# Kernel optimization log

Hardware: AMD Instinct MI355X
Metric: run time of the kernel (lower is better)

The kernel has to match this reference:

```python
import jax, jax.numpy as jnp
import numpy as np

TEMPERATURE = 0.07


def setup_inputs() -> dict:
    key = jax.random.key(0)
    k1, k2 = jax.random.split(key)
    B, D = 8192, 128
    z_i = jax.random.normal(k1, (B, D), dtype=jnp.float32)
    z_j = jax.random.normal(k2, (B, D), dtype=jnp.float32)
    return {"z_i": z_i, "z_j": z_j}


def reference(z_i, z_j):
    B = z_i.shape[0]
    # L2-normalize each embedding (F.normalize with eps=1e-12 clamp)
    def l2norm(x):
        n = jnp.linalg.norm(x, axis=1, keepdims=True)
        return x / jnp.maximum(n, 1e-12)
    reps = jnp.concatenate([l2norm(z_i), l2norm(z_j)], axis=0)  # [2B, D]
    sim = jnp.matmul(reps, reps.T) / TEMPERATURE  # [2B, 2B]
    # NOTE: original code applies CrossEntropyLoss to exp(sim/T) values,
    # i.e. the logits themselves are the exponentiated similarities.
    e = jnp.exp(sim)
    N = 2 * B
    idx = jnp.arange(N)
    # CE with the positive placed first and all non-diagonal entries as logits:
    # loss_i = logsumexp(nondiag row) - positive_logit
    neg_inf = jnp.asarray(-jnp.inf, dtype=e.dtype)
    row_logits = jnp.where(idx[None, :] == idx[:, None], neg_inf, e)  # mask diagonal
    lse = jax.scipy.special.logsumexp(row_logits, axis=1)  # [2B]
    pos_idx = jnp.where(idx < B, idx + B, idx - B)
    pos = e[idx, pos_idx]  # [2B]
    return jnp.mean(lse - pos)
```

## Files before the change

### kernel.cpp

```cpp
#include <hip/hip_runtime.h>
#include <hip/hip_bf16.h>


#define NROWS 16384
#define BHALF 8192
#define DDIM  128
#define TILE  128
#define ROWS_PER_BLOCK 256
#define NSPLIT 8
#define COLS_PER_SPLIT (NROWS / NSPLIT)
#define NITERS (COLS_PER_SPLIT / TILE)
#define LDS_STRIDE 136
#define LOG2E 1.4426950408889634f
#define C_EXP (LOG2E / 0.07f)
#define NEGBIG -1.0e30f

typedef __attribute__((ext_vector_type(8))) short bf16x8;
typedef __attribute__((ext_vector_type(4))) float f32x4;

__device__ inline unsigned short f2bf(float x) {
    unsigned int b = __float_as_uint(x);
    b += 0x7FFFu + ((b >> 16) & 1u);
    return (unsigned short)(b >> 16);
}
__device__ inline float bflo(unsigned int u) { return __uint_as_float(u << 16); }
__device__ inline float bfhi(unsigned int u) { return __uint_as_float(u & 0xFFFF0000u); }

__global__ void norm_kernel(const float* __restrict__ zi, const float* __restrict__ zj,
                            unsigned short* __restrict__ repsB,
                            unsigned short* __restrict__ repsA,
                            float* __restrict__ out) {
    int w = threadIdx.x >> 6;
    int lane = threadIdx.x & 63;
    int row = blockIdx.x * 4 + w;
    const float* src = (row < BHALF) ? (zi + (size_t)row * DDIM)
                                     : (zj + (size_t)(row - BHALF) * DDIM);
    float2 v = ((const float2*)src)[lane];
    float ss = v.x * v.x + v.y * v.y;
    #pragma unroll
    for (int d = 1; d < 64; d <<= 1) ss += __shfl_xor(ss, d, 64);
    float inv = 1.0f / fmaxf(sqrtf(ss), 1e-12f);
    float x = v.x * inv, y = v.y * inv;
    unsigned int pb = (unsigned int)f2bf(x) | ((unsigned int)f2bf(y) << 16);
    unsigned int pa = (unsigned int)f2bf(x * C_EXP) | ((unsigned int)f2bf(y * C_EXP) << 16);
    ((unsigned int*)repsB)[(size_t)row * (DDIM / 2) + lane] = pb;
    ((unsigned int*)repsA)[(size_t)row * (DDIM / 2) + lane] = pa;
    if (blockIdx.x == 0 && threadIdx.x == 0) out[0] = 0.0f;
}

template <bool DIAG>
__device__ __forceinline__ void tile_compute(const unsigned short* lds,
                                             const bf16x8 (&afrag)[4][4],
                                             float (&A1)[4][4], float (&A2)[4][4],
                                             int rowBase, int colBase,
                                             int laneLo, int quad) {
    #pragma unroll
    for (int c8 = 0; c8 < 8; ++c8) {
        bf16x8 bfrag[4];
        int brow = c8 * 16 + laneLo;
        #pragma unroll
        for (int kt = 0; kt < 4; ++kt)
            bfrag[kt] = *(const bf16x8*)(&lds[brow * LDS_STRIDE + kt * 32 + quad * 8]);
        #pragma unroll
        for (int rt = 0; rt < 4; ++rt) {
            f32x4 acc = (f32x4){0.f, 0.f, 0.f, 0.f};
            #pragma unroll
            for (int kt = 0; kt < 4; ++kt)
                acc = __builtin_amdgcn_mfma_f32_16x16x32_bf16(
                    afrag[rt][kt], bfrag[kt], acc, 0, 0, 0);
            #pragma unroll
            for (int rg = 0; rg < 4; ++rg) {
                float a = acc[rg];
                if (DIAG) {
                    int drel = rowBase + rt * 16 + quad * 4 + rg - colBase - laneLo;
                    a = (drel == c8 * 16) ? NEGBIG : a;
                }
                float mn = fminf(a, A1[rt][rg]);
                A2[rt][rg] = fmaxf(A2[rt][rg], mn);
                A1[rt][rg] = fmaxf(A1[rt][rg], a);
            }
        }
    }
}

__global__ __launch_bounds__(256, 2)
void ntx_main(const unsigned short* __restrict__ repsA,
              const unsigned short* __restrict__ repsB,
              float2* __restrict__ part) {
    __shared__ unsigned short lds[TILE * LDS_STRIDE];
    const int tid = threadIdx.x;
    const int w = tid >> 6, lane = tid & 63;
    const int laneLo = lane & 15, quad = lane >> 4;
    const int bx = blockIdx.x, by = blockIdx.y;
    const int rowBase = bx * ROWS_PER_BLOCK + w * 64;

    bf16x8 afrag[4][4];
    #pragma unroll
    for (int rt = 0; rt < 4; ++rt)
        #pragma unroll
        for (int kt = 0; kt < 4; ++kt) {
            int r = rowBase + rt * 16 + laneLo;
            int k = kt * 32 + quad * 8;
            afrag[rt][kt] = *(const bf16x8*)(repsA + (size_t)r * DDIM + k);
        }

    float A1[4][4], A2[4][4];
    #pragma unroll
    for (int rt = 0; rt < 4; ++rt)
        #pragma unroll
        for (int rg = 0; rg < 4; ++rg) { A1[rt][rg] = NEGBIG; A2[rt][rg] = NEGBIG; }

    const int colBase0 = by * COLS_PER_SPLIT;
    const uint4* repsV = (const uint4*)repsB;

    for (int it = 0; it < NITERS; ++it) {
        int colBase = colBase0 + it * TILE;
        __syncthreads();
        #pragma unroll
        for (int i = 0; i < 8; ++i) {
            int idx = tid + i * 256;
            int r = idx >> 4, c = idx & 15;
            uint4 v = repsV[(size_t)(colBase + r) * 16 + c];
            *(uint4*)(&lds[r * LDS_STRIDE + c * 8]) = v;
        }
        __syncthreads();

        if ((rowBase >> 7) == (colBase >> 7))
            tile_compute<true>(lds, afrag, A1, A2, rowBase, colBase, laneLo, quad);
        else
            tile_compute<false>(lds, afrag, A1, A2, rowBase, colBase, laneLo, quad);
    }

    #pragma unroll
    for (int rt = 0; rt < 4; ++rt)
        #pragma unroll
        for (int rg = 0; rg < 4; ++rg) {
            float m1 = A1[rt][rg], m2 = A2[rt][rg];
            #pragma unroll
            for (int d = 1; d < 16; d <<= 1) {
                float m1o = __shfl_xor(m1, d, 64);
                float m2o = __shfl_xor(m2, d, 64);
                m2 = fmaxf(fmaxf(m2, m2o), fminf(m1, m1o));
                m1 = fmaxf(m1, m1o);
            }
            if (laneLo == 0) {
                int gr = rowBase + rt * 16 + quad * 4 + rg;
                part[(size_t)gr * NSPLIT + by] = make_float2(m1, m2);
            }
        }
}

__global__ void finish_kernel(const unsigned short* __restrict__ repsB,
                              const float2* __restrict__ part,
                              float* __restrict__ out) {
    int row = blockIdx.x * 256 + threadIdx.x;
    int prow = (row < BHALF) ? row + BHALF : row - BHALF;
    const uint4* rv = (const uint4*)repsB + (size_t)row * 16;
    const uint4* pv = (const uint4*)repsB + (size_t)prow * 16;
    float dot = 0.0f;
    #pragma unroll
    for (int c = 0; c < 16; ++c) {
        uint4 a = rv[c], b = pv[c];
        dot = fmaf(bflo(a.x), bflo(b.x), dot); dot = fmaf(bfhi(a.x), bfhi(b.x), dot);
        dot = fmaf(bflo(a.y), bflo(b.y), dot); dot = fmaf(bfhi(a.y), bfhi(b.y), dot);
        dot = fmaf(bflo(a.z), bflo(b.z), dot); dot = fmaf(bfhi(a.z), bfhi(b.z), dot);
        dot = fmaf(bflo(a.w), bflo(b.w), dot); dot = fmaf(bfhi(a.w), bfhi(b.w), dot);
    }
    float pos = __builtin_amdgcn_exp2f(dot * C_EXP);

    float M1 = NEGBIG, M2 = NEGBIG;
    #pragma unroll
    for (int k = 0; k < NSPLIT; ++k) {
        float2 p = part[(size_t)row * NSPLIT + k];
        M2 = fmaxf(fmaxf(M2, p.y), fminf(M1, p.x));
        M1 = fmaxf(M1, p.x);
    }
    float e1 = __builtin_amdgcn_exp2f(M1);
    float e2 = __builtin_amdgcn_exp2f(M2);
    float lse = e1 + log1pf(__builtin_amdgcn_exp2f((e2 - e1) * LOG2E));
    float v = lse - pos;

    #pragma unroll
    for (int d = 1; d < 64; d <<= 1) v += __shfl_xor(v, d, 64);
    __shared__ float red[4];
    int lane = threadIdx.x & 63, w = threadIdx.x >> 6;
    if (lane == 0) red[w] = v;
    __syncthreads();
    if (threadIdx.x == 0)
        atomicAdd(out, (red[0] + red[1] + red[2] + red[3]) * (1.0f / NROWS));
}

extern "C" void kernel_launch(void* const* d_in, const int* in_sizes, int n_in,
                              void* d_out, int out_size, void* d_ws, size_t ws_size,
                              hipStream_t stream) {
    const float* zi = (const float*)d_in[0];
    const float* zj = (const float*)d_in[1];
    float* out = (float*)d_out;
    unsigned short* repsB = (unsigned short*)d_ws;
    unsigned short* repsA = repsB + (size_t)NROWS * DDIM;
    float2* part = (float2*)((char*)d_ws + 2 * (size_t)NROWS * DDIM * 2);

    norm_kernel<<<NROWS / 4, 256, 0, stream>>>(zi, zj, repsB, repsA, out);
    ntx_main<<<dim3(NROWS / ROWS_PER_BLOCK, NSPLIT), 256, 0, stream>>>(repsA, repsB, part);
    finish_kernel<<<NROWS / 256, 256, 0, stream>>>(repsB, part, out);
}
```

Measured before the change: 137.5 us.

## Widen column tile, interleave two MFMA chains, fuse positive extraction into main kernel

```diff
diff --git a/kernel.cpp b/kernel.cpp
--- a/kernel.cpp
+++ b/kernel.cpp
@@ -5,7 +5,7 @@
 #define NROWS 16384
 #define BHALF 8192
 #define DDIM  128
-#define TILE  128
+#define TILE  256
 #define ROWS_PER_BLOCK 256
 #define NSPLIT 8
 #define COLS_PER_SPLIT (NROWS / NSPLIT)
@@ -23,8 +23,6 @@
     b += 0x7FFFu + ((b >> 16) & 1u);
     return (unsigned short)(b >> 16);
 }
-__device__ inline float bflo(unsigned int u) { return __uint_as_float(u << 16); }
-__device__ inline float bfhi(unsigned int u) { return __uint_as_float(u & 0xFFFF0000u); }
 
 __global__ void norm_kernel(const float* __restrict__ zi, const float* __restrict__ zj,
                             unsigned short* __restrict__ repsB,
@@ -48,36 +46,47 @@
     if (blockIdx.x == 0 && threadIdx.x == 0) out[0] = 0.0f;
 }
 
-template <bool DIAG>
-__device__ __forceinline__ void tile_compute(const unsigned short* lds,
-                                             const bf16x8 (&afrag)[4][4],
-                                             float (&A1)[4][4], float (&A2)[4][4],
-                                             int rowBase, int colBase,
-                                             int laneLo, int quad) {
-    #pragma unroll
-    for (int c8 = 0; c8 < 8; ++c8) {
-        bf16x8 bfrag[4];
-        int brow = c8 * 16 + laneLo;
-        #pragma unroll
-        for (int kt = 0; kt < 4; ++kt)
-            bfrag[kt] = *(const bf16x8*)(&lds[brow * LDS_STRIDE + kt * 32 + quad * 8]);
+template <int MODE>
+__device__ __forceinline__ void tile_compute(
+    const unsigned short* __restrict__ lds,
+    const bf16x8 (&afrag)[4][4],
+    float (&A1)[4][4], float (&A2)[4][4], float (&POS)[4][4],
+    int rowOff, int laneLo, int quad) {
+    const f32x4 kZ = {0.f, 0.f, 0.f, 0.f};
+    #pragma unroll
+    for (int c8 = 0; c8 < 16; c8 += 2) {
+        bf16x8 ba[4], bb[4];
+        const int browa = c8 * 16 + laneLo;
+        #pragma unroll
+        for (int kt = 0; kt < 4; ++kt) {
+            ba[kt] = *(const bf16x8*)(&lds[browa * LDS_STRIDE + kt * 32 + quad * 8]);
+            bb[kt] = *(const bf16x8*)(&lds[(browa + 16) * LDS_STRIDE + kt * 32 + quad * 8]);
+        }
         #pragma unroll
         for (int rt = 0; rt < 4; ++rt) {
-            f32x4 acc = (f32x4){0.f, 0.f, 0.f, 0.f};
+            f32x4 va = kZ, vb = kZ;
             #pragma unroll
-            for (int kt = 0; kt < 4; ++kt)
-                acc = __builtin_amdgcn_mfma_f32_16x16x32_bf16(
-                    afrag[rt][kt], bfrag[kt], acc, 0, 0, 0);
+            for (int kt = 0; kt < 4; ++kt) {
+                va = __builtin_amdgcn_mfma_f32_16x16x32_bf16(afrag[rt][kt], ba[kt], va, 0, 0, 0);
+                vb = __builtin_amdgcn_mfma_f32_16x16x32_bf16(afrag[rt][kt], bb[kt], vb, 0, 0, 0);
+            }
             #pragma unroll
             for (int rg = 0; rg < 4; ++rg) {
-                float a = acc[rg];
-                if (DIAG) {
-                    int drel = rowBase + rt * 16 + quad * 4 + rg - colBase - laneLo;
-                    a = (drel == c8 * 16) ? NEGBIG : a;
+                float a = va[rg], b = vb[rg];
+                if (MODE) {
+                    int rel = rowOff + rt * 16 + quad * 4 + rg - laneLo;
+                    if (MODE == 1) {
+                        a = (rel == c8 * 16) ? NEGBIG : a;
+                        b = (rel == (c8 + 1) * 16) ? NEGBIG : b;
+                    } else {
+                        POS[rt][rg] = fmaxf(POS[rt][rg], (rel == c8 * 16) ? a : NEGBIG);
+                        POS[rt][rg] = fmaxf(POS[rt][rg], (rel == (c8 + 1) * 16) ? b : NEGBIG);
+                    }
                 }
-                float mn = fminf(a, A1[rt][rg]);
-                A2[rt][rg] = fmaxf(A2[rt][rg], mn);
-                A1[rt][rg] = fmaxf(A1[rt][rg], a);
+                float hi = fmaxf(a, b), lo = fminf(a, b);
+                float t = fminf(A1[rt][rg], hi);
+                A1[rt][rg] = fmaxf(A1[rt][rg], hi);
+                A2[rt][rg] = fmaxf(fmaxf(A2[rt][rg], lo), t);
             }
         }
     }
@@ -86,13 +95,17 @@
 __global__ __launch_bounds__(256, 2)
 void ntx_main(const unsigned short* __restrict__ repsA,
               const unsigned short* __restrict__ repsB,
-              float2* __restrict__ part) {
+              float4* __restrict__ part) {
     __shared__ unsigned short lds[TILE * LDS_STRIDE];
     const int tid = threadIdx.x;
     const int w = tid >> 6, lane = tid & 63;
     const int laneLo = lane & 15, quad = lane >> 4;
     const int bx = blockIdx.x, by = blockIdx.y;
     const int rowBase = bx * ROWS_PER_BLOCK + w * 64;
+    const int rowOff = rowBase & 255;
+
+    const int diagCol = bx * ROWS_PER_BLOCK;
+    const int posCol = (diagCol < BHALF) ? diagCol + BHALF : diagCol - BHALF;
 
     bf16x8 afrag[4][4];
     #pragma unroll
@@ -104,11 +117,13 @@
             afrag[rt][kt] = *(const bf16x8*)(repsA + (size_t)r * DDIM + k);
         }
 
-    float A1[4][4], A2[4][4];
+    float A1[4][4], A2[4][4], POS[4][4];
     #pragma unroll
     for (int rt = 0; rt < 4; ++rt)
         #pragma unroll
-        for (int rg = 0; rg < 4; ++rg) { A1[rt][rg] = NEGBIG; A2[rt][rg] = NEGBIG; }
+        for (int rg = 0; rg < 4; ++rg) {
+            A1[rt][rg] = NEGBIG; A2[rt][rg] = NEGBIG; POS[rt][rg] = NEGBIG;
+        }
 
     const int colBase0 = by * COLS_PER_SPLIT;
     const uint4* repsV = (const uint4*)repsB;
@@ -117,7 +132,7 @@
         int colBase = colBase0 + it * TILE;
         __syncthreads();
         #pragma unroll
-        for (int i = 0; i < 8; ++i) {
+        for (int i = 0; i < 16; ++i) {
             int idx = tid + i * 256;
             int r = idx >> 4, c = idx & 15;
             uint4 v = repsV[(size_t)(colBase + r) * 16 + c];
@@ -125,58 +140,49 @@
         }
         __syncthreads();
 
-        if ((rowBase >> 7) == (colBase >> 7))
-            tile_compute<true>(lds, afrag, A1, A2, rowBase, colBase, laneLo, quad);
+        if (colBase == diagCol)
+            tile_compute<1>(lds, afrag, A1, A2, POS, rowOff, laneLo, quad);
+        else if (colBase == posCol)
+            tile_compute<2>(lds, afrag, A1, A2, POS, rowOff, laneLo, quad);
         else
-            tile_compute<false>(lds, afrag, A1, A2, rowBase, colBase, laneLo, quad);
+            tile_compute<0>(lds, afrag, A1, A2, POS, rowOff, laneLo, quad);
     }
 
     #pragma unroll
     for (int rt = 0; rt < 4; ++rt)
         #pragma unroll
         for (int rg = 0; rg < 4; ++rg) {
-            float m1 = A1[rt][rg], m2 = A2[rt][rg];
+            float m1 = A1[rt][rg], m2 = A2[rt][rg], p = POS[rt][rg];
             #pragma unroll
             for (int d = 1; d < 16; d <<= 1) {
                 float m1o = __shfl_xor(m1, d, 64);
                 float m2o = __shfl_xor(m2, d, 64);
+                float po = __shfl_xor(p, d, 64);
                 m2 = fmaxf(fmaxf(m2, m2o), fminf(m1, m1o));
                 m1 = fmaxf(m1, m1o);
+                p = fmaxf(p, po);
             }
             if (laneLo == 0) {
                 int gr = rowBase + rt * 16 + quad * 4 + rg;
-                part[(size_t)gr * NSPLIT + by] = make_float2(m1, m2);
-            }
-        }
-}
-
-__global__ void finish_kernel(const unsigned short* __restrict__ repsB,
-                              const float2* __restrict__ part,
+                part[(size_t)gr * NSPLIT + by] = make_float4(m1, m2, p, 0.0f);
+            }
+        }
+}
+
+__global__ void finish_kernel(const float4* __restrict__ part,
                               float* __restrict__ out) {
     int row = blockIdx.x * 256 + threadIdx.x;
-    int prow = (row < BHALF) ? row + BHALF : row - BHALF;
-    const uint4* rv = (const uint4*)repsB + (size_t)row * 16;
-    const uint4* pv = (const uint4*)repsB + (size_t)prow * 16;
-    float dot = 0.0f;
-    #pragma unroll
-    for (int c = 0; c < 16; ++c) {
-        uint4 a = rv[c], b = pv[c];
-        dot = fmaf(bflo(a.x), bflo(b.x), dot); dot = fmaf(bfhi(a.x), bfhi(b.x), dot);
-        dot = fmaf(bflo(a.y), bflo(b.y), dot); dot = fmaf(bfhi(a.y), bfhi(b.y), dot);
-        dot = fmaf(bflo(a.z), bflo(b.z), dot); dot = fmaf(bfhi(a.z), bfhi(b.z), dot);
-        dot = fmaf(bflo(a.w), bflo(b.w), dot); dot = fmaf(bfhi(a.w), bfhi(b.w), dot);
-    }
-    float pos = __builtin_amdgcn_exp2f(dot * C_EXP);
-
-    float M1 = NEGBIG, M2 = NEGBIG;
+    float M1 = NEGBIG, M2 = NEGBIG, P = NEGBIG;
     #pragma unroll
     for (int k = 0; k < NSPLIT; ++k) {
-        float2 p = part[(size_t)row * NSPLIT + k];
+        float4 p = part[(size_t)row * NSPLIT + k];
         M2 = fmaxf(fmaxf(M2, p.y), fminf(M1, p.x));
         M1 = fmaxf(M1, p.x);
+        P = fmaxf(P, p.z);
     }
     float e1 = __builtin_amdgcn_exp2f(M1);
     float e2 = __builtin_amdgcn_exp2f(M2);
+    float pos = __builtin_amdgcn_exp2f(P);
     float lse = e1 + log1pf(__builtin_amdgcn_exp2f((e2 - e1) * LOG2E));
     float v = lse - pos;
 
@@ -198,9 +204,9 @@
     float* out = (float*)d_out;
     unsigned short* repsB = (unsigned short*)d_ws;
     unsigned short* repsA = repsB + (size_t)NROWS * DDIM;
-    float2* part = (float2*)((char*)d_ws + 2 * (size_t)NROWS * DDIM * 2);
+    float4* part = (float4*)((char*)d_ws + 2 * (size_t)NROWS * DDIM * 2);
 
     norm_kernel<<<NROWS / 4, 256, 0, stream>>>(zi, zj, repsB, repsA, out);
     ntx_main<<<dim3(NROWS / ROWS_PER_BLOCK, NSPLIT), 256, 0, stream>>>(repsA, repsB, part);
-    finish_kernel<<<NROWS / 256, 256, 0, stream>>>(repsB, part, out);
-}
+    finish_kernel<<<NROWS / 256, 256, 0, stream>>>(part, out);
+}
```

Measured after the change: 150.9 us. 1.1x slower.

## Double-buffer LDS column tiles with register prefetch in similarity kernel

Applied to the files above, without the earlier changes.

```diff
diff --git a/kernel.cpp b/kernel.cpp
--- a/kernel.cpp
+++ b/kernel.cpp
@@ -49,7 +49,7 @@
 }
 
 template <bool DIAG>
-__device__ __forceinline__ void tile_compute(const unsigned short* lds,
+__device__ __forceinline__ void tile_compute(const unsigned short* __restrict__ lds,
                                              const bf16x8 (&afrag)[4][4],
                                              float (&A1)[4][4], float (&A2)[4][4],
                                              int rowBase, int colBase,
@@ -87,7 +87,7 @@
 void ntx_main(const unsigned short* __restrict__ repsA,
               const unsigned short* __restrict__ repsB,
               float2* __restrict__ part) {
-    __shared__ unsigned short lds[TILE * LDS_STRIDE];
+    __shared__ unsigned short lds[2][TILE * LDS_STRIDE];
     const int tid = threadIdx.x;
     const int w = tid >> 6, lane = tid & 63;
     const int laneLo = lane & 15, quad = lane >> 4;
@@ -112,23 +112,34 @@
 
     const int colBase0 = by * COLS_PER_SPLIT;
     const uint4* repsV = (const uint4*)repsB;
-
+    const int r0 = tid >> 4, c0 = tid & 15;
+
+    uint4 pf[8];
+    #pragma unroll
+    for (int i = 0; i < 8; ++i)
+        pf[i] = repsV[(size_t)(colBase0 + r0 + i * 16) * 16 + c0];
+    #pragma unroll
+    for (int i = 0; i < 8; ++i)
+        *(uint4*)(&lds[0][(r0 + i * 16) * LDS_STRIDE + c0 * 8]) = pf[i];
+
+    int buf = 0;
     for (int it = 0; it < NITERS; ++it) {
+        __syncthreads();
         int colBase = colBase0 + it * TILE;
-        __syncthreads();
-        #pragma unroll
-        for (int i = 0; i < 8; ++i) {
-            int idx = tid + i * 256;
-            int r = idx >> 4, c = idx & 15;
-            uint4 v = repsV[(size_t)(colBase + r) * 16 + c];
-            *(uint4*)(&lds[r * LDS_STRIDE + c * 8]) = v;
-        }
-        __syncthreads();
+        int nextCol = colBase0 + ((it + 1) & (NITERS - 1)) * TILE;
+        #pragma unroll
+        for (int i = 0; i < 8; ++i)
+            pf[i] = repsV[(size_t)(nextCol + r0 + i * 16) * 16 + c0];
 
         if ((rowBase >> 7) == (colBase >> 7))
-            tile_compute<true>(lds, afrag, A1, A2, rowBase, colBase, laneLo, quad);
+            tile_compute<true>(lds[buf], afrag, A1, A2, rowBase, colBase, laneLo, quad);
         else
-            tile_compute<false>(lds, afrag, A1, A2, rowBase, colBase, laneLo, quad);
+            tile_compute<false>(lds[buf], afrag, A1, A2, rowBase, colBase, laneLo, quad);
+
+        #pragma unroll
+        for (int i = 0; i < 8; ++i)
+            *(uint4*)(&lds[buf ^ 1][(r0 + i * 16) * LDS_STRIDE + c0 * 8]) = pf[i];
+        buf ^= 1;
     }
 
     #pragma unroll
```

Measured after the change: 137.3 us. About the same (-0.2%).

## Load B fragments directly from global memory instead of staging through LDS

Applied to the files above, without the earlier changes.

```diff
diff --git a/kernel.cpp b/kernel.cpp
--- a/kernel.cpp
+++ b/kernel.cpp
@@ -10,7 +10,6 @@
 #define NSPLIT 8
 #define COLS_PER_SPLIT (NROWS / NSPLIT)
 #define NITERS (COLS_PER_SPLIT / TILE)
-#define LDS_STRIDE 136
 #define LOG2E 1.4426950408889634f
 #define C_EXP (LOG2E / 0.07f)
 #define NEGBIG -1.0e30f
@@ -49,18 +48,17 @@
 }
 
 template <bool DIAG>
-__device__ __forceinline__ void tile_compute(const unsigned short* lds,
+__device__ __forceinline__ void tile_compute(const unsigned short* __restrict__ bptr,
                                              const bf16x8 (&afrag)[4][4],
                                              float (&A1)[4][4], float (&A2)[4][4],
-                                             int rowBase, int colBase,
-                                             int laneLo, int quad) {
+                                             int drel0, int quad) {
     #pragma unroll
     for (int c8 = 0; c8 < 8; ++c8) {
         bf16x8 bfrag[4];
-        int brow = c8 * 16 + laneLo;
+        const unsigned short* p = bptr + (size_t)(c8 * 16) * DDIM;
         #pragma unroll
         for (int kt = 0; kt < 4; ++kt)
-            bfrag[kt] = *(const bf16x8*)(&lds[brow * LDS_STRIDE + kt * 32 + quad * 8]);
+            bfrag[kt] = *(const bf16x8*)(p + kt * 32);
         #pragma unroll
         for (int rt = 0; rt < 4; ++rt) {
             f32x4 acc = (f32x4){0.f, 0.f, 0.f, 0.f};
@@ -72,7 +70,7 @@
             for (int rg = 0; rg < 4; ++rg) {
                 float a = acc[rg];
                 if (DIAG) {
-                    int drel = rowBase + rt * 16 + quad * 4 + rg - colBase - laneLo;
+                    int drel = drel0 + rt * 16 + quad * 4 + rg;
                     a = (drel == c8 * 16) ? NEGBIG : a;
                 }
                 float mn = fminf(a, A1[rt][rg]);
@@ -87,7 +85,6 @@
 void ntx_main(const unsigned short* __restrict__ repsA,
               const unsigned short* __restrict__ repsB,
               float2* __restrict__ part) {
-    __shared__ unsigned short lds[TILE * LDS_STRIDE];
     const int tid = threadIdx.x;
     const int w = tid >> 6, lane = tid & 63;
     const int laneLo = lane & 15, quad = lane >> 4;
@@ -111,24 +108,16 @@
         for (int rg = 0; rg < 4; ++rg) { A1[rt][rg] = NEGBIG; A2[rt][rg] = NEGBIG; }
 
     const int colBase0 = by * COLS_PER_SPLIT;
-    const uint4* repsV = (const uint4*)repsB;
+    const int drel0 = rowBase - laneLo;
 
     for (int it = 0; it < NITERS; ++it) {
         int colBase = colBase0 + it * TILE;
-        __syncthreads();
-        #pragma unroll
-        for (int i = 0; i < 8; ++i) {
-            int idx = tid + i * 256;
-            int r = idx >> 4, c = idx & 15;
-            uint4 v = repsV[(size_t)(colBase + r) * 16 + c];
-            *(uint4*)(&lds[r * LDS_STRIDE + c * 8]) = v;
-        }
-        __syncthreads();
-
+        const unsigned short* bptr =
+            repsB + (size_t)(colBase + laneLo) * DDIM + quad * 8;
         if ((rowBase >> 7) == (colBase >> 7))
-            tile_compute<true>(lds, afrag, A1, A2, rowBase, colBase, laneLo, quad);
+            tile_compute<true>(bptr, afrag, A1, A2, drel0 - colBase, quad);
         else
-            tile_compute<false>(lds, afrag, A1, A2, rowBase, colBase, laneLo, quad);
+            tile_compute<false>(bptr, afrag, A1, A2, 0, quad);
     }
 
     #pragma unroll
```

After: 187.8 us. 1.37x slower.
